# Performance work log

Hardware: AMD Instinct MI355X
Metric: run time of the kernel (lower is better)

The kernel has to match this reference:

```python
import jax, jax.numpy as jnp
import numpy as np

B = 2097152   # batch
L = 5         # latent_size
H = 16        # mlp_size
P = 2         # param_size
CLS = 3       # closure input size: concat([Y, x1, x2])


def _init_linear(key, fan_in, fan_out):
    kw, kb = jax.random.split(key)
    bound = 1.0 / np.sqrt(fan_in)
    W = jax.random.uniform(kw, (fan_in, fan_out), jnp.float32, -bound, bound)
    b = jax.random.uniform(kb, (fan_out,), jnp.float32, -bound, bound)
    return W, b


def setup_inputs() -> dict:
    key = jax.random.key(0)
    ks = jax.random.split(key, 10)
    inputs = jax.random.normal(ks[0], (B, 2), jnp.float32)
    Z = jax.random.normal(ks[1], (B, L), jnp.float32)
    Y = jax.random.normal(ks[2], (B, 1), jnp.float32)
    # nn.Parameter(torch.zeros(L, L)) in the original; use small random so the
    # matmul path is numerically non-trivial for kernel testing.
    A = jax.random.normal(ks[3], (L, L), jnp.float32) * 0.1
    w2a, b2a = _init_linear(ks[4], L, H)
    w2b, b2b = _init_linear(ks[5], H, H)
    w2c, b2c = _init_linear(ks[6], H, P)
    wfa, bfa = _init_linear(ks[7], CLS, H)
    wfb, bfb = _init_linear(ks[8], H, H)
    wfc, bfc = _init_linear(ks[9], H, 1)
    return dict(inputs=inputs, Z=Z, Y=Y, A=A,
                w2a=w2a, b2a=b2a, w2b=w2b, b2b=b2b, w2c=w2c, b2c=b2c,
                wfa=wfa, bfa=bfa, wfb=wfb, bfb=bfb, wfc=wfc, bfc=bfc)


def reference(inputs, Z, Y, A, w2a, b2a, w2b, b2b, w2c, b2c,
              wfa, bfa, wfb, bfb, wfc, bfc):
    x1 = inputs[:, 0:1]
    x2 = inputs[:, 1:2]
    c = 0.0  # self.switch defaults to 0

    new_Z = Z @ A                                   # [B, L]
    # mlp2: L -> H -> H -> P with ReLU on hidden layers
    h = jax.nn.relu(new_Z @ w2a + b2a)
    h = jax.nn.relu(h @ w2b + b2b)
    K = jnp.abs(h @ w2c + b2c)                      # [B, P]
    k1 = K[:, 0:1]
    k2 = K[:, 1:2]

    # closure MLP f[0]: concat([Y, x1, x2]) -> 1 (multiplied by switch c)
    fin = jnp.concatenate([Y, x1, x2], axis=-1)     # [B, 3]
    g = jax.nn.relu(fin @ wfa + bfa)
    g = jax.nn.relu(g @ wfb + bfb)
    g = g @ wfc + bfc                               # [B, 1]

    DY = -Y + k1 * x1 - k2 * x2 + c * g
    new_S = Y + DY
    # original returns (Y + DY, [new_Z, new_S])
    return (new_S, new_Z, new_S)
```

## Files before the change

kernel.cpp:

```cpp
#include <hip/hip_runtime.h>


#define LDIM 5
#define HDIM 16
constexpr int BLOCK = 256;

typedef float f32x2 __attribute__((ext_vector_type(2)));

__device__ __forceinline__ f32x2 fma2(f32x2 a, f32x2 b, f32x2 c) {
    return __builtin_elementwise_fma(a, b, c);
}
__device__ __forceinline__ f32x2 max2(f32x2 a, f32x2 b) {
    return __builtin_elementwise_max(a, b);
}

__global__ __launch_bounds__(BLOCK, 8) void lpsc_main(
    const float* __restrict__ inputs,
    const float* __restrict__ Zin,
    const float* __restrict__ Yin,
    const float* __restrict__ A,
    const float* __restrict__ w2a, const float* __restrict__ b2a,
    const float* __restrict__ w2b, const float* __restrict__ b2b,
    const float* __restrict__ w2c, const float* __restrict__ b2c,
    float* __restrict__ out,
    unsigned B)
{
    const unsigned row = blockIdx.x * (unsigned)BLOCK + threadIdx.x;
    if (row >= B) return;

    const f32x2* W1 = reinterpret_cast<const f32x2*>(w2a);
    const f32x2* B1 = reinterpret_cast<const f32x2*>(b2a);
    const f32x2* W2 = reinterpret_cast<const f32x2*>(w2b);
    const f32x2* B2 = reinterpret_cast<const f32x2*>(b2b);
    const f32x2* W3 = reinterpret_cast<const f32x2*>(w2c);
    const f32x2  b3 = *reinterpret_cast<const f32x2*>(b2c);

    const f32x2 xv = reinterpret_cast<const f32x2*>(inputs)[row];
    const float y = Yin[row];
    float z[LDIM];
    #pragma unroll
    for (int k = 0; k < LDIM; ++k) z[k] = Zin[(size_t)row * LDIM + k];

    float nz[LDIM];
    #pragma unroll
    for (int j = 0; j < LDIM; ++j) nz[j] = 0.0f;
    #pragma unroll
    for (int k = 0; k < LDIM; ++k)
        #pragma unroll
        for (int j = 0; j < LDIM; ++j)
            nz[j] = fmaf(z[k], A[k * LDIM + j], nz[j]);

    f32x2 h[HDIM / 2];
    #pragma unroll
    for (int jp = 0; jp < HDIM / 2; ++jp) h[jp] = B1[jp];
    #pragma unroll
    for (int k = 0; k < LDIM; ++k) {
        const f32x2 a2 = {nz[k], nz[k]};
        #pragma unroll
        for (int jp = 0; jp < HDIM / 2; ++jp)
            h[jp] = fma2(a2, W1[k * (HDIM / 2) + jp], h[jp]);
    }
    const f32x2 zero = {0.0f, 0.0f};
    #pragma unroll
    for (int jp = 0; jp < HDIM / 2; ++jp) h[jp] = max2(h[jp], zero);

    f32x2 g2[HDIM / 2];
    #pragma unroll
    for (int jp = 0; jp < HDIM / 2; ++jp) g2[jp] = B2[jp];
    #pragma unroll
    for (int k = 0; k < HDIM; ++k) {
        const float hk = (k & 1) ? h[k >> 1].y : h[k >> 1].x;
        const f32x2 a2 = {hk, hk};
        #pragma unroll
        for (int jp = 0; jp < HDIM / 2; ++jp)
            g2[jp] = fma2(a2, W2[k * (HDIM / 2) + jp], g2[jp]);
    }
    #pragma unroll
    for (int jp = 0; jp < HDIM / 2; ++jp) g2[jp] = max2(g2[jp], zero);

    f32x2 k12 = b3;
    #pragma unroll
    for (int k = 0; k < HDIM; ++k) {
        const float gk = (k & 1) ? g2[k >> 1].y : g2[k >> 1].x;
        const f32x2 a2 = {gk, gk};
        k12 = fma2(a2, W3[k], k12);
    }

    const float K1 = fabsf(k12.x);
    const float K2 = fabsf(k12.y);
    const float ns = y + (-y + K1 * xv.x - K2 * xv.y);

    out[row] = ns;
    out[(size_t)6 * B + row] = ns;
    float* oz = out + (size_t)B + (size_t)row * LDIM;
    #pragma unroll
    for (int j = 0; j < LDIM; ++j) oz[j] = nz[j];
}

extern "C" void kernel_launch(void* const* d_in, const int* in_sizes, int n_in,
                              void* d_out, int out_size, void* d_ws, size_t ws_size,
                              hipStream_t stream) {
    const float* inputs = (const float*)d_in[0];
    const float* Zin    = (const float*)d_in[1];
    const float* Yin    = (const float*)d_in[2];
    const float* A      = (const float*)d_in[3];
    const float* w2a    = (const float*)d_in[4];
    const float* b2a    = (const float*)d_in[5];
    const float* w2b    = (const float*)d_in[6];
    const float* b2b    = (const float*)d_in[7];
    const float* w2c    = (const float*)d_in[8];
    const float* b2c    = (const float*)d_in[9];

    const unsigned B = (unsigned)in_sizes[2];
    const unsigned grid = (B + BLOCK - 1) / BLOCK;

    lpsc_main<<<grid, BLOCK, 0, stream>>>(inputs, Zin, Yin, A, w2a, b2a,
                                          w2b, b2b, w2c, b2c,
                                          (float*)d_out, B);
}
```

Baseline: 142.3 us.

## Use persistent grid-stride loop with register double-buffered row prefetch

Replaces the one-row-per-thread launch with a fixed grid of 2048 blocks that stride over the batch. Each thread prefetches the next row's inputs into a second register set while it computes and stores the current row, so load latency overlaps the MLP arithmetic. The cost is more live registers (the occupancy hint of 8 was dropped from the launch bounds) and a fixed grid that may not match the device's CU count.

New measurement: 169.4 us. 19.0% more time.

```diff
diff --git a/kernel.cpp b/kernel.cpp
--- a/kernel.cpp
+++ b/kernel.cpp
@@ -4,6 +4,7 @@
 #define LDIM 5
 #define HDIM 16
 constexpr int BLOCK = 256;
+constexpr int GRID  = 2048;
 
 typedef float f32x2 __attribute__((ext_vector_type(2)));
 
@@ -14,32 +15,31 @@
     return __builtin_elementwise_max(a, b);
 }
 
-__global__ __launch_bounds__(BLOCK, 8) void lpsc_main(
-    const float* __restrict__ inputs,
-    const float* __restrict__ Zin,
-    const float* __restrict__ Yin,
+struct RowIn {
+    f32x2 xv;
+    float y;
+    float z0, z1, z2, z3, z4;
+};
+
+__device__ __forceinline__ void load_row(const float* __restrict__ inputs,
+                                         const float* __restrict__ Zin,
+                                         const float* __restrict__ Yin,
+                                         unsigned row, RowIn& R) {
+    R.xv = reinterpret_cast<const f32x2*>(inputs)[row];
+    R.y  = Yin[row];
+    const float* zr = Zin + (size_t)row * LDIM;
+    R.z0 = zr[0]; R.z1 = zr[1]; R.z2 = zr[2]; R.z3 = zr[3]; R.z4 = zr[4];
+}
+
+__device__ __forceinline__ void compute_store(
+    const RowIn& R, unsigned row,
     const float* __restrict__ A,
-    const float* __restrict__ w2a, const float* __restrict__ b2a,
-    const float* __restrict__ w2b, const float* __restrict__ b2b,
-    const float* __restrict__ w2c, const float* __restrict__ b2c,
-    float* __restrict__ out,
-    unsigned B)
+    const f32x2* __restrict__ W1, const f32x2* __restrict__ B1,
+    const f32x2* __restrict__ W2, const f32x2* __restrict__ B2,
+    const f32x2* __restrict__ W3, f32x2 b3,
+    float* __restrict__ out, unsigned B)
 {
-    const unsigned row = blockIdx.x * (unsigned)BLOCK + threadIdx.x;
-    if (row >= B) return;
-
-    const f32x2* W1 = reinterpret_cast<const f32x2*>(w2a);
-    const f32x2* B1 = reinterpret_cast<const f32x2*>(b2a);
-    const f32x2* W2 = reinterpret_cast<const f32x2*>(w2b);
-    const f32x2* B2 = reinterpret_cast<const f32x2*>(b2b);
-    const f32x2* W3 = reinterpret_cast<const f32x2*>(w2c);
-    const f32x2  b3 = *reinterpret_cast<const f32x2*>(b2c);
-
-    const f32x2 xv = reinterpret_cast<const f32x2*>(inputs)[row];
-    const float y = Yin[row];
-    float z[LDIM];
-    #pragma unroll
-    for (int k = 0; k < LDIM; ++k) z[k] = Zin[(size_t)row * LDIM + k];
+    float z[LDIM] = {R.z0, R.z1, R.z2, R.z3, R.z4};
 
     float nz[LDIM];
     #pragma unroll
@@ -88,13 +88,51 @@
 
     const float K1 = fabsf(k12.x);
     const float K2 = fabsf(k12.y);
-    const float ns = y + (-y + K1 * xv.x - K2 * xv.y);
+    const float ns = R.y + (-R.y + K1 * R.xv.x - K2 * R.xv.y);
 
     out[row] = ns;
     out[(size_t)6 * B + row] = ns;
     float* oz = out + (size_t)B + (size_t)row * LDIM;
-    #pragma unroll
-    for (int j = 0; j < LDIM; ++j) oz[j] = nz[j];
+    oz[0] = nz[0]; oz[1] = nz[1]; oz[2] = nz[2]; oz[3] = nz[3]; oz[4] = nz[4];
+}
+
+__global__ __launch_bounds__(BLOCK) void lpsc_main(
+    const float* __restrict__ inputs,
+    const float* __restrict__ Zin,
+    const float* __restrict__ Yin,
+    const float* __restrict__ A,
+    const float* __restrict__ w2a, const float* __restrict__ b2a,
+    const float* __restrict__ w2b, const float* __restrict__ b2b,
+    const float* __restrict__ w2c, const float* __restrict__ b2c,
+    float* __restrict__ out,
+    unsigned B)
+{
+    const f32x2* W1 = reinterpret_cast<const f32x2*>(w2a);
+    const f32x2* B1 = reinterpret_cast<const f32x2*>(b2a);
+    const f32x2* W2 = reinterpret_cast<const f32x2*>(w2b);
+    const f32x2* B2 = reinterpret_cast<const f32x2*>(b2b);
+    const f32x2* W3 = reinterpret_cast<const f32x2*>(w2c);
+    const f32x2  b3 = *reinterpret_cast<const f32x2*>(b2c);
+
+    const unsigned S = (unsigned)GRID * BLOCK;
+    unsigned ra = blockIdx.x * (unsigned)BLOCK + threadIdx.x;
+    if (ra >= B) return;
+
+    RowIn RA, RB;
+    load_row(inputs, Zin, Yin, ra, RA);
+    unsigned rb = ra + S;
+
+    for (;;) {
+        if (rb < B) load_row(inputs, Zin, Yin, rb, RB);
+        compute_store(RA, ra, A, W1, B1, W2, B2, W3, b3, out, B);
+        if (rb >= B) return;
+
+        ra = rb + S;
+        if (ra < B) load_row(inputs, Zin, Yin, ra, RA);
+        compute_store(RB, rb, A, W1, B1, W2, B2, W3, b3, out, B);
+        if (ra >= B) return;
+        rb = ra + S;
+    }
 }
 
 extern "C" void kernel_launch(void* const* d_in, const int* in_sizes, int n_in,
@@ -112,7 +150,9 @@
     const float* b2c    = (const float*)d_in[9];
 
     const unsigned B = (unsigned)in_sizes[2];
-    const unsigned grid = (B + BLOCK - 1) / BLOCK;
+    unsigned grid = GRID;
+    const unsigned needed = (B + BLOCK - 1) / BLOCK;
+    if (needed < grid) grid = needed;
 
     lpsc_main<<<grid, BLOCK, 0, stream>>>(inputs, Zin, Yin, A, w2a, b2a,
                                           w2b, b2b, w2c, b2c,
```
